# Kernel optimization log

Hardware: AMD Instinct MI355X
Metric: run time of the kernel (lower is better)

The kernel has to match this reference:

```python
import jax, jax.numpy as jnp
import numpy as np

EPS = 1e-6

def _ln(x, g, b):
    m = x.mean(-1, keepdims=True)
    v = jnp.var(x, axis=-1, keepdims=True)
    return (x - m) * jax.lax.rsqrt(v + EPS) * g + b

def _mha(x, qkv_w, out_w, out_b, heads, dh):
    # vit-style attention: Linear(dim, 3*heads*dh, bias=False), chunk into q,k,v
    B, N, _ = x.shape
    qkv = (x @ qkv_w).reshape(B, N, 3, heads, dh).transpose(2, 0, 3, 1, 4)
    q, k, v = qkv[0], qkv[1], qkv[2]                       # [B,H,N,dh]
    attn = jax.nn.softmax(jnp.einsum('bhid,bhjd->bhij', q, k) * (dh ** -0.5), axis=-1)
    o = jnp.einsum('bhij,bhjd->bhid', attn, v).transpose(0, 2, 1, 3).reshape(B, N, heads * dh)
    return o @ out_w + out_b

def _tx(x, p, heads, dh):
    # standard prenorm transformer stack, p = stacked per-layer params
    (l1g, l1b, qw, ow, ob, l2g, l2b, f1w, f1b, f2w, f2b, ng, nb) = p
    for i in range(l1g.shape[0]):
        x = x + _mha(_ln(x, l1g[i], l1b[i]), qw[i], ow[i], ob[i], heads, dh)
        h = _ln(x, l2g[i], l2b[i])
        x = x + jax.nn.gelu(h @ f1w[i] + f1b[i]) @ f2w[i] + f2b[i]
    return _ln(x, ng, nb)

def _ats(x, l1g, l1b, qkvw, qkvb, projw, projb, l2g, l2b, f1w, f1b, f2w, f2b):
    # ATS block: attention + CLS-significance-driven adaptive token resampling (gather)
    B, N, D = x.shape
    heads = 6
    dh = D // heads
    h = _ln(x, l1g, l1b)
    qkv = (h @ qkvw + qkvb).reshape(B, N, 3, heads, dh).transpose(2, 0, 3, 1, 4)
    q, k, v = qkv[0], qkv[1], qkv[2]
    attn = jax.nn.softmax(jnp.einsum('bhid,bhjd->bhij', q, k) * (dh ** -0.5), axis=-1)  # [B,H,N,N]
    y = jnp.einsum('bhij,bhjd->bhid', attn, v).transpose(0, 2, 1, 3).reshape(B, N, D)
    y = y @ projw + projb
    # significance score: cls attention * value norm (ATS, Fayyaz et al.)
    vn = jnp.linalg.norm(v, axis=-1)                        # [B,H,N]
    s = (attn[:, :, 0, 1:] * vn[:, :, 1:]).mean(axis=1)     # [B,N-1]
    s = s / (s.sum(-1, keepdims=True) + 1e-8)
    cdf = jnp.cumsum(s, axis=-1)                            # [B,N-1]
    # deterministic inverse-transform sampling of N-1 tokens
    u = (jnp.arange(N - 1, dtype=x.dtype) + 0.5) / (N - 1)
    idx = jax.vmap(lambda c: jnp.searchsorted(c, u))(cdf)
    idx = jnp.clip(idx, 0, N - 2) + 1                       # skip cls slot
    idx = jnp.concatenate([jnp.zeros((B, 1), idx.dtype), idx], axis=1)  # keep cls
    g = lambda a: jnp.take_along_axis(a, idx[:, :, None], axis=1)
    x = g(x) + g(y)
    h = _ln(x, l2g, l2b)
    return x + jax.nn.gelu(h @ f1w + f1b) @ f2w + f2b

def reference(x, patch_w, patch_b, pos_emb, space_token, temporal_token,
              s_ln1_g, s_ln1_b, s_qkv_w, s_out_w, s_out_b, s_ln2_g, s_ln2_b,
              s_fc1_w, s_fc1_b, s_fc2_w, s_fc2_b, s_norm_g, s_norm_b,
              t_ln1_g, t_ln1_b, t_qkv_w, t_out_w, t_out_b, t_ln2_g, t_ln2_b,
              t_fc1_w, t_fc1_b, t_fc2_w, t_fc2_b, t_norm_g, t_norm_b,
              a_ln1_g, a_ln1_b, a_qkv_w, a_qkv_b, a_proj_w, a_proj_b,
              a_ln2_g, a_ln2_b, a_fc1_w, a_fc1_b, a_fc2_w, a_fc2_b,
              final_g, final_b, h1_w, h1_b, h2_w, h2_b):
    B, T = x.shape[0], x.shape[1]
    BT, D, P, HP = B * T, 192, 16, 14
    # patch embedding (conv16s16 as unfold + linear), channel-major flattening
    xt = x.reshape(BT, 3, HP, P, HP, P).transpose(0, 2, 4, 1, 3, 5).reshape(BT, HP * HP, 3 * P * P)
    xt = (xt @ patch_w + patch_b).reshape(B, T, HP * HP, D)
    cls = jnp.broadcast_to(space_token.reshape(1, 1, 1, D), (B, T, 1, D))
    xt = jnp.concatenate([cls, xt], axis=2) + pos_emb      # [B,T,197,D]
    xt = xt.reshape(BT, 197, D)
    xt = _tx(xt, (s_ln1_g, s_ln1_b, s_qkv_w, s_out_w, s_out_b, s_ln2_g, s_ln2_b,
                  s_fc1_w, s_fc1_b, s_fc2_w, s_fc2_b, s_norm_g, s_norm_b), 6, 64)
    for i in range(a_ln1_g.shape[0]):
        xt = _ats(xt, a_ln1_g[i], a_ln1_b[i], a_qkv_w[i], a_qkv_b[i], a_proj_w[i],
                  a_proj_b[i], a_ln2_g[i], a_ln2_b[i], a_fc1_w[i], a_fc1_b[i],
                  a_fc2_w[i], a_fc2_b[i])
    xc = xt[:, 0].reshape(B, T, D)
    tt = jnp.broadcast_to(temporal_token, (B, 1, D))
    xc = jnp.concatenate([tt, xc], axis=1)                 # [B,T+1,D]
    xc = _tx(xc, (t_ln1_g, t_ln1_b, t_qkv_w, t_out_w, t_out_b, t_ln2_g, t_ln2_b,
                  t_fc1_w, t_fc1_b, t_fc2_w, t_fc2_b, t_norm_g, t_norm_b), 6, 64)
    f = jnp.max(xc, axis=1)                                # AdaptiveMaxPool1d(1) over tokens
    f = _ln(f, final_g, final_b)
    return jax.nn.relu(f @ h1_w + h1_b) @ h2_w + h2_b      # mlp_head -> [B,2]

def setup_inputs():
    key = jax.random.key(0)
    ks = iter(jax.random.split(key, 64))
    def rn(shape, s=0.02):
        return jax.random.normal(next(ks), shape, dtype=jnp.float32) * s
    d = {}
    d['x'] = jax.random.normal(next(ks), (16, 5, 3, 224, 224), dtype=jnp.float32)
    d['patch_w'] = rn((768, 192)); d['patch_b'] = jnp.zeros((192,), jnp.float32)
    d['pos_emb'] = rn((1, 5, 197, 192))
    d['space_token'] = rn((1, 1, 192)); d['temporal_token'] = rn((1, 1, 192))
    def tx(depth, n):
        d[n + '_ln1_g'] = jnp.ones((depth, 192), jnp.float32); d[n + '_ln1_b'] = jnp.zeros((depth, 192), jnp.float32)
        d[n + '_qkv_w'] = rn((depth, 192, 1152)); d[n + '_out_w'] = rn((depth, 384, 192)); d[n + '_out_b'] = jnp.zeros((depth, 192), jnp.float32)
        d[n + '_ln2_g'] = jnp.ones((depth, 192), jnp.float32); d[n + '_ln2_b'] = jnp.zeros((depth, 192), jnp.float32)
        d[n + '_fc1_w'] = rn((depth, 192, 768)); d[n + '_fc1_b'] = jnp.zeros((depth, 768), jnp.float32)
        d[n + '_fc2_w'] = rn((depth, 768, 192)); d[n + '_fc2_b'] = jnp.zeros((depth, 192), jnp.float32)
        d[n + '_norm_g'] = jnp.ones((192,), jnp.float32); d[n + '_norm_b'] = jnp.zeros((192,), jnp.float32)
    tx(2, 's'); tx(3, 't')
    d['a_ln1_g'] = jnp.ones((12, 192), jnp.float32); d['a_ln1_b'] = jnp.zeros((12, 192), jnp.float32)
    d['a_qkv_w'] = rn((12, 192, 576)); d['a_qkv_b'] = jnp.zeros((12, 576), jnp.float32)
    d['a_proj_w'] = rn((12, 192, 192)); d['a_proj_b'] = jnp.zeros((12, 192), jnp.float32)
    d['a_ln2_g'] = jnp.ones((12, 192), jnp.float32); d['a_ln2_b'] = jnp.zeros((12, 192), jnp.float32)
    d['a_fc1_w'] = rn((12, 192, 768)); d['a_fc1_b'] = jnp.zeros((12, 768), jnp.float32)
    d['a_fc2_w'] = rn((12, 768, 192)); d['a_fc2_b'] = jnp.zeros((12, 192), jnp.float32)
    d['final_g'] = jnp.ones((192,), jnp.float32); d['final_b'] = jnp.zeros((192,), jnp.float32)
    d['h1_w'] = rn((192, 64)); d['h1_b'] = jnp.zeros((64,), jnp.float32)
    d['h2_w'] = rn((64, 2)); d['h2_b'] = jnp.zeros((2,), jnp.float32)
    return d
```

## Files before the change

### kernel.cpp

```cpp
#include <hip/hip_runtime.h>
#include <hip/hip_bf16.h>
#include <math.h>

typedef float in_t;
typedef float out_t;

__device__ __forceinline__ float ldi(const in_t* p, size_t i) { return (float)p[i]; }

#define DMODEL 192
#define NTOK   197
#define BT_    80
#define ROWS_  (BT_*NTOK)

__device__ __forceinline__ float gelu_f(float v) {
  return 0.5f*v*(1.f + tanhf(0.7978845608028654f*(v + 0.044715f*v*v*v)));
}

__device__ __forceinline__ short f2bf(float f) {
  union { float f; unsigned u; } v; v.f = f;
  unsigned r = v.u + 0x7FFFu + ((v.u >> 16) & 1u);
  return (short)(r >> 16);
}

typedef __attribute__((ext_vector_type(8))) short bfrag;
typedef __attribute__((ext_vector_type(4))) float f32x4;

__global__ __launch_bounds__(256)
void wconv_k(const float* __restrict__ W, short* __restrict__ O, int K, int N)
{
  __shared__ float tile[32][33];
  const int l = blockIdx.z;
  const int k0 = blockIdx.y*32, n0 = blockIdx.x*32;
  const float* Wl = W + (size_t)l*K*N;
  short* Ol = O + (size_t)l*K*N;
  const int tx = threadIdx.x & 31, ty = threadIdx.x >> 5;
  #pragma unroll
  for (int r = ty; r < 32; r += 8) {
    int k = k0 + r, n = n0 + tx;
    tile[r][tx] = (k < K && n < N) ? Wl[(size_t)k*N + n] : 0.f;
  }
  __syncthreads();
  #pragma unroll
  for (int r = ty; r < 32; r += 8) {
    int n = n0 + r, k = k0 + tx;
    if (n < N && k < K) Ol[(size_t)n*K + k] = f2bf(tile[tx][r]);
  }
}

template<int EPI, int ABF, int OBF>
__global__ __launch_bounds__(256)
void gemmW_k(const void* __restrict__ Ain, const short* __restrict__ Wt,
             const float* __restrict__ bias, const float* __restrict__ R,
             void* __restrict__ Cout, int M, int N, int K)
{
  constexpr int LP = 200;
  __shared__ short Asb[64][LP];
  __shared__ short Bsb[64][LP];
  const int t = threadIdx.x;
  const int w = t >> 6, lane = t & 63;
  const int bm0 = blockIdx.y*64, bn0 = blockIdx.x*64;
  const int sr = t >> 2;
  const int sk = (t & 3) * 8;
  f32x4 acc[4] = {};

  for (int k0 = 0; k0 < K; k0 += 192) {
    const int gm = bm0 + sr;
    #pragma unroll
    for (int cc = 0; cc < 6; ++cc) {
      const int kk = cc*32 + sk;
      short y[8] = {0,0,0,0,0,0,0,0};
      if (gm < M) {
        if (ABF == 0) {
          const float* ap = (const float*)Ain + (size_t)gm*K + k0 + kk;
          float4 v0 = *(const float4*)ap;
          float4 v1 = *(const float4*)(ap + 4);
          y[0]=f2bf(v0.x); y[1]=f2bf(v0.y); y[2]=f2bf(v0.z); y[3]=f2bf(v0.w);
          y[4]=f2bf(v1.x); y[5]=f2bf(v1.y); y[6]=f2bf(v1.z); y[7]=f2bf(v1.w);
        } else {
          *(bfrag*)y = *(const bfrag*)((const short*)Ain + (size_t)gm*K + k0 + kk);
        }
      }
      *(bfrag*)&Asb[sr][kk] = *(bfrag*)y;
      bfrag bv = *(const bfrag*)(Wt + (size_t)(bn0 + sr)*K + k0 + kk);
      *(bfrag*)&Bsb[sr][kk] = bv;
    }
    __syncthreads();
    const int fr = lane & 15, g8 = (lane >> 4) * 8;
    #pragma unroll
    for (int ks = 0; ks < 6; ++ks) {
      bfrag af = *(const bfrag*)&Asb[w*16 + fr][ks*32 + g8];
      #pragma unroll
      for (int nt = 0; nt < 4; ++nt) {
        bfrag bf = *(const bfrag*)&Bsb[nt*16 + fr][ks*32 + g8];
        acc[nt] = __builtin_amdgcn_mfma_f32_16x16x32_bf16(af, bf, acc[nt], 0, 0, 0);
      }
    }
    __syncthreads();
  }
  const int col = lane & 15, rg = (lane >> 4) * 4;
  #pragma unroll
  for (int nt = 0; nt < 4; ++nt) {
    int gn = bn0 + nt*16 + col;
    float bv = bias ? bias[gn] : 0.f;
    #pragma unroll
    for (int r = 0; r < 4; ++r) {
      int gm = bm0 + w*16 + rg + r;
      if (gm < M) {
        float v = acc[nt][r] + bv;
        if (EPI==1) v = gelu_f(v);
        if (EPI==2) v += R[(size_t)gm*N + gn];
        if (OBF) ((short*)Cout)[(size_t)gm*N + gn] = f2bf(v);
        else     ((float*)Cout)[(size_t)gm*N + gn] = v;
      }
    }
  }
}

__global__ __launch_bounds__(256)
void ln_k(const float* __restrict__ x, const in_t* __restrict__ g, const in_t* __restrict__ b,
          float* __restrict__ o, int rows)
{
  int t = threadIdx.x, wave = t>>6, lane = t&63;
  int r = blockIdx.x*4 + wave;
  if (r >= rows) return;
  const float* xr = x + (size_t)r*DMODEL;
  float e0 = xr[lane], e1 = xr[lane+64], e2 = xr[lane+128];
  float s = e0+e1+e2;
  #pragma unroll
  for (int off=32; off; off>>=1) s += __shfl_xor(s, off);
  float mean = s / 192.f;
  float d0=e0-mean, d1=e1-mean, d2=e2-mean;
  float v = d0*d0+d1*d1+d2*d2;
  #pragma unroll
  for (int off=32; off; off>>=1) v += __shfl_xor(v, off);
  float rs = 1.f / sqrtf(v/192.f + 1e-6f);
  float* orow = o + (size_t)r*DMODEL;
  orow[lane]     = d0*rs*ldi(g,lane)     + ldi(b,lane);
  orow[lane+64]  = d1*rs*ldi(g,lane+64)  + ldi(b,lane+64);
  orow[lane+128] = d2*rs*ldi(g,lane+128) + ldi(b,lane+128);
}

template<int DH, int W>
__global__ __launch_bounds__(W*64)
void attnM_k(const float* __restrict__ qkv, short* __restrict__ out,
             float* __restrict__ attn0, int heads, float scale)
{
  constexpr int NSEQ = 197;
  constexpr int NP   = 224;
  constexpr int KG   = DH/8;
  constexpr int CT   = DH/16;
  constexpr int NF   = DH/32;
  __shared__ short Kb[KG][NP][8];
  __shared__ short Vt[NP/8][DH][8];
  __shared__ short Ps[W][NP/8][16][8];

  const int bh = blockIdx.x;
  const int b = bh / heads, h = bh - b*heads;
  const int stride = 3*heads*DH;
  const float* __restrict__ base = qkv + (size_t)b*NSEQ*stride;
  const int qo = h*DH, ko = heads*DH + h*DH, vo = 2*heads*DH + h*DH;
  const int t = threadIdx.x, w = t>>6, lane = t&63;

  for (int idx = t; idx < NP*DH; idx += W*64) {
    int j = idx / DH, d = idx - j*DH;
    float kv = 0.f, vv = 0.f;
    if (j < NSEQ) {
      kv = base[(size_t)j*stride + ko + d];
      vv = base[(size_t)j*stride + vo + d];
    }
    Kb[d>>3][j][d&7] = f2bf(kv);
    Vt[j>>3][d][j&7] = f2bf(vv);
  }
  __syncthreads();

  const int c = lane & 15, g = lane >> 4, rg = g*4;
  const float NEG = -3.0e38f;

  for (int st = w; st < 13; st += W) {
    const int q0 = st*16;
    int qrow = q0 + c; if (qrow > NSEQ-1) qrow = NSEQ-1;
    bfrag aq[NF];
    {
      const float* qp = base + (size_t)qrow*stride + qo + g*8;
      #pragma unroll
      for (int f = 0; f < NF; ++f) {
        float4 v0 = *(const float4*)(qp + f*32);
        float4 v1 = *(const float4*)(qp + f*32 + 4);
        short y[8] = {f2bf(v0.x),f2bf(v0.y),f2bf(v0.z),f2bf(v0.w),
                      f2bf(v1.x),f2bf(v1.y),f2bf(v1.z),f2bf(v1.w)};
        aq[f] = *(bfrag*)y;
      }
    }
    f32x4 sacc[14];
    #pragma unroll
    for (int jt = 0; jt < 14; ++jt) sacc[jt] = (f32x4){0.f,0.f,0.f,0.f};
    #pragma unroll
    for (int jt = 0; jt < 13; ++jt) {
      #pragma unroll
      for (int f = 0; f < NF; ++f) {
        bfrag bk = *(const bfrag*)&Kb[f*4 + g][jt*16 + c][0];
        sacc[jt] = __builtin_amdgcn_mfma_f32_16x16x32_bf16(aq[f], bk, sacc[jt], 0, 0, 0);
      }
    }
    float m0[4] = {NEG,NEG,NEG,NEG};
    #pragma unroll
    for (int jt = 0; jt < 14; ++jt) {
      const bool valid = (jt < 13) && (jt*16 + c < NSEQ);
      #pragma unroll
      for (int r = 0; r < 4; ++r) {
        float sv = valid ? sacc[jt][r]*scale : NEG;
        sacc[jt][r] = sv;
        m0[r] = fmaxf(m0[r], sv);
      }
    }
    #pragma unroll
    for (int off = 1; off < 16; off <<= 1)
      #pragma unroll
      for (int r = 0; r < 4; ++r) m0[r] = fmaxf(m0[r], __shfl_xor(m0[r], off));
    float sum[4] = {0.f,0.f,0.f,0.f};
    #pragma unroll
    for (int jt = 0; jt < 14; ++jt)
      #pragma unroll
      for (int r = 0; r < 4; ++r) {
        float e = expf(sacc[jt][r] - m0[r]);
        sacc[jt][r] = e;
        sum[r] += e;
      }
    #pragma unroll
    for (int off = 1; off < 16; off <<= 1)
      #pragma unroll
      for (int r = 0; r < 4; ++r) sum[r] += __shfl_xor(sum[r], off);
    float inv[4];
    #pragma unroll
    for (int r = 0; r < 4; ++r) inv[r] = 1.f / sum[r];

    if (attn0 != nullptr && st == 0 && g == 0) {
      #pragma unroll
      for (int jt = 0; jt < 13; ++jt) {
        int j = jt*16 + c;
        if (j < NSEQ) attn0[(size_t)bh*NSEQ + j] = sacc[jt][0]*inv[0];
      }
    }
    #pragma unroll
    for (int jt = 0; jt < 14; ++jt)
      #pragma unroll
      for (int r = 0; r < 4; ++r)
        Ps[w][jt*2 + (c>>3)][rg + r][c&7] = f2bf(sacc[jt][r]);
    f32x4 oacc[CT];
    #pragma unroll
    for (int ct = 0; ct < CT; ++ct) oacc[ct] = (f32x4){0.f,0.f,0.f,0.f};
    #pragma unroll
    for (int kc = 0; kc < 7; ++kc) {
      bfrag ap = *(const bfrag*)&Ps[w][kc*4 + g][c][0];
      #pragma unroll
      for (int ct = 0; ct < CT; ++ct) {
        bfrag bv = *(const bfrag*)&Vt[kc*4 + g][ct*16 + c][0];
        oacc[ct] = __builtin_amdgcn_mfma_f32_16x16x32_bf16(ap, bv, oacc[ct], 0, 0, 0);
      }
    }
    #pragma unroll
    for (int ct = 0; ct < CT; ++ct)
      #pragma unroll
      for (int r = 0; r < 4; ++r) {
        int q = q0 + rg + r;
        if (q < NSEQ)
          out[((size_t)b*NSEQ + q)*(size_t)(heads*DH) + h*DH + ct*16 + c] = f2bf(oacc[ct][r]*inv[r]);
      }
  }
}

template<int DH, int W>
__global__ __launch_bounds__(W*64)
void attn2r_k(const float* __restrict__ qkv, float* __restrict__ out,
              float* __restrict__ attn0, int Nseq, int heads, float scale)
{
  constexpr int QT = 8;
  constexpr int KTS = 204;
  constexpr int NPART = (DH == 64) ? 1 : 2;
  constexpr int DQ   = DH/4;
  constexpr int QPG  = 2;
  __shared__ float Kt[DH * KTS];
  __shared__ float Qt[W][DH][12];
  __shared__ float Ps[W][QT][200];

  const int bh = blockIdx.x;
  const int b = bh / heads, h = bh % heads;
  const int stride = 3 * heads * DH;
  const float* __restrict__ base = qkv + (size_t)b * Nseq * stride;
  const int qo = h * DH, ko = heads * DH + h * DH, vo = 2 * heads * DH + h * DH;
  const int t = threadIdx.x, w = t >> 6, lane = t & 63;

  for (int idx = t; idx < Nseq * DH; idx += W * 64) {
    int j = idx / DH, d0 = idx - j * DH;
    Kt[d0 * KTS + j] = base[(size_t)j * stride + ko + d0];
  }
  __syncthreads();

  const int d = lane & (DH - 1);
  const int nchunks = (Nseq + QT - 1) / QT;
  const int jcmax = (Nseq + 3) >> 2;
  const float NEG = -3.0e38f;
  const float4* Kt4 = (const float4*)Kt;

  const int part = (NPART == 2) ? (lane >> 5) : 0;
  const int qg   = (DH == 64) ? (lane >> 4) : ((lane >> 3) & 3);
  const int dq   = lane & (DQ - 1);
  const int dv   = 4 * dq;

  for (int ic = w; ic < nchunks; ic += W) {
    const int i0 = ic * QT;
    if ((DH == 64) || (lane >> 5) == 0) {
      #pragma unroll
      for (int q = 0; q < QT; ++q) {
        int i = i0 + q;
        Qt[w][d][q] = (i < Nseq) ? base[(size_t)i * stride + qo + d] : 0.f;
      }
    }
    float s[QT][4];
    #pragma unroll
    for (int q = 0; q < QT; ++q)
      #pragma unroll
      for (int u = 0; u < 4; ++u) s[q][u] = 0.f;
    #pragma unroll 4
    for (int dd = 0; dd < DH; ++dd) {
      float4 kv = (lane < 51) ? Kt4[dd * (KTS/4) + lane] : make_float4(0.f,0.f,0.f,0.f);
      float4 qA = *(const float4*)&Qt[w][dd][0];
      float4 qB = *(const float4*)&Qt[w][dd][4];
      float qv[8] = {qA.x, qA.y, qA.z, qA.w, qB.x, qB.y, qB.z, qB.w};
      float kr[4] = {kv.x, kv.y, kv.z, kv.w};
      #pragma unroll
      for (int q = 0; q < QT; ++q)
        #pragma unroll
        for (int u = 0; u < 4; ++u)
          s[q][u] = fmaf(qv[q], kr[u], s[q][u]);
    }
    float inv[QT];
    #pragma unroll
    for (int q = 0; q < QT; ++q) {
      float mx = NEG;
      #pragma unroll
      for (int u = 0; u < 4; ++u) {
        int j = 4*lane + u;
        s[q][u] = (j < Nseq) ? s[q][u]*scale : NEG;
        mx = fmaxf(mx, s[q][u]);
      }
      #pragma unroll
      for (int off = 32; off; off >>= 1) mx = fmaxf(mx, __shfl_xor(mx, off));
      float sum = 0.f;
      #pragma unroll
      for (int u = 0; u < 4; ++u) {
        float p = (4*lane + u < Nseq) ? expf(s[q][u] - mx) : 0.f;
        s[q][u] = p; sum += p;
      }
      #pragma unroll
      for (int off = 32; off; off >>= 1) sum += __shfl_xor(sum, off);
      inv[q] = 1.f / sum;
      if (lane < 50)
        *(float4*)&Ps[w][q][4*lane] = make_float4(s[q][0], s[q][1], s[q][2], s[q][3]);
    }
    if (attn0 != nullptr && i0 == 0) {
      #pragma unroll
      for (int u = 0; u < 4; ++u) {
        int j = 4*lane + u;
        if (j < Nseq) attn0[(size_t)bh*Nseq + j] = s[0][u]*inv[0];
      }
    }
    float o[QPG][4];
    #pragma unroll
    for (int qi = 0; qi < QPG; ++qi) { o[qi][0]=0.f; o[qi][1]=0.f; o[qi][2]=0.f; o[qi][3]=0.f; }
    const float* __restrict__ Vg = base + vo;
    for (int jc = part; jc < jcmax; jc += NPART) {
      const int jb = 4*jc;
      float4 V0 = make_float4(0.f,0.f,0.f,0.f), V1=V0, V2=V0, V3=V0;
      if (jb+0 < Nseq) V0 = *(const float4*)&Vg[(size_t)(jb+0)*stride + dv];
      if (jb+1 < Nseq) V1 = *(const float4*)&Vg[(size_t)(jb+1)*stride + dv];
      if (jb+2 < Nseq) V2 = *(const float4*)&Vg[(size_t)(jb+2)*stride + dv];
      if (jb+3 < Nseq) V3 = *(const float4*)&Vg[(size_t)(jb+3)*stride + dv];
      #pragma unroll
      for (int qi = 0; qi < QPG; ++qi) {
        float4 p4 = *(const float4*)&Ps[w][qg*QPG+qi][jb];
        o[qi][0] = fmaf(p4.w,V3.x, fmaf(p4.z,V2.x, fmaf(p4.y,V1.x, fmaf(p4.x,V0.x, o[qi][0]))));
        o[qi][1] = fmaf(p4.w,V3.y, fmaf(p4.z,V2.y, fmaf(p4.y,V1.y, fmaf(p4.x,V0.y, o[qi][1]))));
        o[qi][2] = fmaf(p4.w,V3.z, fmaf(p4.z,V2.z, fmaf(p4.y,V1.z, fmaf(p4.x,V0.z, o[qi][2]))));
        o[qi][3] = fmaf(p4.w,V3.w, fmaf(p4.z,V2.w, fmaf(p4.y,V1.w, fmaf(p4.x,V0.w, o[qi][3]))));
      }
    }
    if (NPART == 2) {
      #pragma unroll
      for (int qi = 0; qi < QPG; ++qi) {
        o[qi][0] += __shfl_xor(o[qi][0], 32);
        o[qi][1] += __shfl_xor(o[qi][1], 32);
        o[qi][2] += __shfl_xor(o[qi][2], 32);
        o[qi][3] += __shfl_xor(o[qi][3], 32);
      }
    }
    if (part == 0) {
      #pragma unroll
      for (int qi = 0; qi < QPG; ++qi) {
        float iv = inv[qi];
        if (qg == 1) iv = inv[QPG + qi];
        if (qg == 2) iv = inv[2*QPG + qi];
        if (qg == 3) iv = inv[3*QPG + qi];
        int i = i0 + qg*QPG + qi;
        if (i < Nseq) {
          float4 r = make_float4(o[qi][0]*iv, o[qi][1]*iv, o[qi][2]*iv, o[qi][3]*iv);
          *(float4*)&out[((size_t)b*Nseq + i)*(size_t)(heads*DH) + h*DH + dv] = r;
        }
      }
    }
  }
}

__global__ void patchify_k(const in_t* __restrict__ x, short* __restrict__ A)
{
  int idx = blockIdx.x*256 + threadIdx.x;
  const int total = BT_*196*768;
  if (idx >= total) return;
  int kc = idx % 768;
  int m  = idx / 768;
  int p  = m % 196;
  int bt = m / 196;
  int c  = kc >> 8;
  int py = (kc >> 4) & 15;
  int px = kc & 15;
  int ph = p / 14, pw = p % 14;
  size_t src = (((size_t)bt*3 + c)*224 + (ph*16+py))*224 + (pw*16+px);
  A[idx] = f2bf(ldi(x, src));
}

__global__ void assemble_k(const float* __restrict__ pt, const in_t* __restrict__ st,
                           const in_t* __restrict__ pe, float* __restrict__ X)
{
  int i = blockIdx.x*256 + threadIdx.x;
  const int total = BT_*NTOK*DMODEL;
  if (i >= total) return;
  int d  = i % DMODEL;
  int n  = (i / DMODEL) % NTOK;
  int bt = i / (DMODEL*NTOK);
  int tt = bt % 5;
  float base = (n == 0) ? ldi(st, d)
                        : pt[((size_t)bt*196 + (n-1))*DMODEL + d];
  X[i] = base + ldi(pe, ((size_t)tt*NTOK + n)*DMODEL + d);
}

__global__ void score_k(const float* __restrict__ attn0, const float* __restrict__ qkv,
                        float* __restrict__ S)
{
  int b = blockIdx.x;
  int jj = threadIdx.x;
  if (jj >= 196) return;
  int j = jj + 1;
  float acc = 0.f;
  #pragma unroll
  for (int h = 0; h < 6; ++h) {
    float a0 = attn0[((size_t)b*6 + h)*NTOK + j];
    const float* v = qkv + ((size_t)b*NTOK + j)*576 + 384 + h*32;
    float ss = 0.f;
    #pragma unroll
    for (int d = 0; d < 32; ++d) ss += v[d]*v[d];
    acc += a0 * sqrtf(ss);
  }
  S[(size_t)b*196 + jj] = acc / 6.0f;
}

__global__ void sample_k(const float* __restrict__ S, int* __restrict__ idxout)
{
  __shared__ float cdf[196];
  int b = blockIdx.x, t = threadIdx.x;
  if (t == 0) {
    float tot = 0.f;
    for (int k = 0; k < 196; ++k) tot += S[(size_t)b*196 + k];
    float denom = tot + 1e-8f;
    float run = 0.f;
    for (int k = 0; k < 196; ++k) { run += S[(size_t)b*196 + k] / denom; cdf[k] = run; }
    idxout[(size_t)b*NTOK] = 0;
  }
  __syncthreads();
  if (t < 196) {
    float u = ((float)t + 0.5f) / 196.0f;
    int cnt = 0;
    for (int k = 0; k < 196; ++k) cnt += (cdf[k] < u) ? 1 : 0;
    int c = cnt > 195 ? 195 : cnt;
    idxout[(size_t)b*NTOK + 1 + t] = c + 1;
  }
}

__global__ void gather_k(const float* __restrict__ X, const float* __restrict__ P,
                         const int* __restrict__ idx, float* __restrict__ Xo)
{
  int i = blockIdx.x*256 + threadIdx.x;
  const int total = BT_*NTOK*DMODEL;
  if (i >= total) return;
  int d  = i % DMODEL;
  int n  = (i / DMODEL) % NTOK;
  int bt = i / (DMODEL*NTOK);
  int src = idx[(size_t)bt*NTOK + n];
  size_t sr = ((size_t)bt*NTOK + src)*DMODEL + d;
  Xo[i] = X[sr] + P[sr];
}

__global__ void build_xc_k(const float* __restrict__ X, const in_t* __restrict__ tt,
                           float* __restrict__ xc)
{
  int i = blockIdx.x*256 + threadIdx.x;
  const int total = 16*6*DMODEL;
  if (i >= total) return;
  int d = i % DMODEL;
  int n = (i / DMODEL) % 6;
  int b = i / (DMODEL*6);
  xc[i] = (n == 0) ? ldi(tt, d)
                   : X[(((size_t)b*5 + (n-1))*NTOK + 0)*DMODEL + d];
}

__global__ __launch_bounds__(256)
void head_k(const float* __restrict__ xc, const in_t* __restrict__ fg, const in_t* __restrict__ fb,
            const in_t* __restrict__ w1, const in_t* __restrict__ b1,
            const in_t* __restrict__ w2, const in_t* __restrict__ b2,
            out_t* __restrict__ outp)
{
  __shared__ float fn[DMODEL];
  __shared__ float hid[64];
  __shared__ float mv[2];
  int b = blockIdx.x, t = threadIdx.x;
  if (t < DMODEL) {
    float m = xc[((size_t)b*6 + 0)*DMODEL + t];
    #pragma unroll
    for (int n = 1; n < 6; ++n) m = fmaxf(m, xc[((size_t)b*6 + n)*DMODEL + t]);
    fn[t] = m;
  }
  __syncthreads();
  if (t == 0) {
    float s = 0.f;
    for (int d = 0; d < DMODEL; ++d) s += fn[d];
    float mean = s / 192.f;
    float v = 0.f;
    for (int d = 0; d < DMODEL; ++d) { float dd = fn[d]-mean; v += dd*dd; }
    mv[0] = mean; mv[1] = 1.f / sqrtf(v/192.f + 1e-6f);
  }
  __syncthreads();
  if (t < DMODEL) fn[t] = (fn[t]-mv[0])*mv[1]*ldi(fg,t) + ldi(fb,t);
  __syncthreads();
  if (t < 64) {
    float a = ldi(b1, t);
    for (int d = 0; d < DMODEL; ++d) a += fn[d]*ldi(w1, (size_t)d*64 + t);
    hid[t] = fmaxf(a, 0.f);
  }
  __syncthreads();
  if (t < 2) {
    float a = ldi(b2, t);
    for (int j = 0; j < 64; ++j) a += hid[j]*ldi(w2, (size_t)j*2 + t);
    outp[(size_t)b*2 + t] = (out_t)a;
  }
}

extern "C" void kernel_launch(void* const* d_in, const int* in_sizes, int n_in,
                              void* d_out, int out_size, void* d_ws, size_t ws_size,
                              hipStream_t stream)
{
  if (n_in < 50) return;
  const in_t* x_in     = (const in_t*)d_in[0];
  const in_t* patch_w  = (const in_t*)d_in[1];
  const in_t* patch_b  = (const in_t*)d_in[2];
  const in_t* pos_emb  = (const in_t*)d_in[3];
  const in_t* space_tk = (const in_t*)d_in[4];
  const in_t* temp_tk  = (const in_t*)d_in[5];
  const in_t* s_ln1_g = (const in_t*)d_in[6];  const in_t* s_ln1_b = (const in_t*)d_in[7];
  const in_t* s_qkv_w = (const in_t*)d_in[8];  const in_t* s_out_w = (const in_t*)d_in[9];
  const in_t* s_out_b = (const in_t*)d_in[10]; const in_t* s_ln2_g = (const in_t*)d_in[11];
  const in_t* s_ln2_b = (const in_t*)d_in[12]; const in_t* s_fc1_w = (const in_t*)d_in[13];
  const in_t* s_fc1_b = (const in_t*)d_in[14]; const in_t* s_fc2_w = (const in_t*)d_in[15];
  const in_t* s_fc2_b = (const in_t*)d_in[16]; const in_t* s_nrm_g = (const in_t*)d_in[17];
  const in_t* s_nrm_b = (const in_t*)d_in[18];
  const in_t* t_ln1_g = (const in_t*)d_in[19]; const in_t* t_ln1_b = (const in_t*)d_in[20];
  const in_t* t_qkv_w = (const in_t*)d_in[21]; const in_t* t_out_w = (const in_t*)d_in[22];
  const in_t* t_out_b = (const in_t*)d_in[23]; const in_t* t_ln2_g = (const in_t*)d_in[24];
  const in_t* t_ln2_b = (const in_t*)d_in[25]; const in_t* t_fc1_w = (const in_t*)d_in[26];
  const in_t* t_fc1_b = (const in_t*)d_in[27]; const in_t* t_fc2_w = (const in_t*)d_in[28];
  const in_t* t_fc2_b = (const in_t*)d_in[29]; const in_t* t_nrm_g = (const in_t*)d_in[30];
  const in_t* t_nrm_b = (const in_t*)d_in[31];
  const in_t* a_ln1_g = (const in_t*)d_in[32]; const in_t* a_ln1_b = (const in_t*)d_in[33];
  const in_t* a_qkv_w = (const in_t*)d_in[34]; const in_t* a_qkv_b = (const in_t*)d_in[35];
  const in_t* a_prj_w = (const in_t*)d_in[36]; const in_t* a_prj_b = (const in_t*)d_in[37];
  const in_t* a_ln2_g = (const in_t*)d_in[38]; const in_t* a_ln2_b = (const in_t*)d_in[39];
  const in_t* a_fc1_w = (const in_t*)d_in[40]; const in_t* a_fc1_b = (const in_t*)d_in[41];
  const in_t* a_fc2_w = (const in_t*)d_in[42]; const in_t* a_fc2_b = (const in_t*)d_in[43];
  const in_t* final_g = (const in_t*)d_in[44]; const in_t* final_b = (const in_t*)d_in[45];
  const in_t* h1_w = (const in_t*)d_in[46];    const in_t* h1_b = (const in_t*)d_in[47];
  const in_t* h2_w = (const in_t*)d_in[48];    const in_t* h2_b = (const in_t*)d_in[49];

  float* ws = (float*)d_ws;
  size_t off = 0;
  auto alloc = [&](size_t nf) { size_t r = off; off += (nf + 63) & ~((size_t)63); return r; };
  size_t oX    = alloc((size_t)ROWS_*DMODEL);
  size_t oX2   = alloc((size_t)ROWS_*DMODEL);
  size_t oH    = alloc((size_t)ROWS_*DMODEL);
  size_t oQKV  = alloc((size_t)ROWS_*1152);
  size_t oY    = alloc((size_t)ROWS_*384);
  size_t oA0   = alloc((size_t)480*NTOK);
  size_t oSB   = alloc((size_t)BT_*196);
  size_t oXC   = alloc((size_t)16*6*DMODEL);
  size_t oIDX  = alloc((size_t)BT_*NTOK);
  size_t oFFt  = alloc((size_t)96*768);
  size_t oWB   = alloc((size_t)4202496 + 64);
  size_t oYb   = alloc((size_t)ROWS_*384/2 + 64);
  size_t oFFb  = alloc((size_t)ROWS_*768/2 + 64);
  if (ws_size < off*sizeof(float)) return;

  float* X   = ws + oX;
  float* X2  = ws + oX2;
  float* H   = ws + oH;
  float* QKV = ws + oQKV;
  float* Y   = ws + oY;
  float* A0  = ws + oA0;
  float* SB  = ws + oSB;
  float* XC  = ws + oXC;
  int*   IDX = (int*)(ws + oIDX);
  float* FFt = ws + oFFt;
  short* WB  = (short*)(ws + oWB);
  short* Yb  = (short*)(ws + oYb);
  short* FFb = (short*)(ws + oFFb);

  size_t wo = 0;
  auto wslot = [&](size_t n){ size_t r = wo; wo += n; return r; };
  size_t wPatch = wslot(147456);
  size_t wSqkv  = wslot(442368);
  size_t wSout  = wslot(147456);
  size_t wSfc1  = wslot(294912);
  size_t wSfc2  = wslot(294912);
  size_t wAqkv  = wslot(1327104);
  size_t wAprj  = wslot(442368);
  size_t wAfc1  = wslot(1769472);
  size_t wAfc2  = wslot(1769472);
  size_t wTqkv  = wslot(663552);
  size_t wTout  = wslot(221184);
  size_t wTfc1  = wslot(442368);
  size_t wTfc2  = wslot(442368);

  auto wconv = [&](const in_t* W, size_t slot, int K, int N, int L) {
    dim3 g(N/32, K/32, L);
    hipLaunchKernelGGL(wconv_k, g, dim3(256), 0, stream, W, WB + slot, K, N);
  };
  wconv(patch_w, wPatch, 768, 192, 1);
  wconv(s_qkv_w, wSqkv, 192, 1152, 2);
  wconv(s_out_w, wSout, 384, 192, 2);
  wconv(s_fc1_w, wSfc1, 192, 768, 2);
  wconv(s_fc2_w, wSfc2, 768, 192, 2);
  wconv(a_qkv_w, wAqkv, 192, 576, 12);
  wconv(a_prj_w, wAprj, 192, 192, 12);
  wconv(a_fc1_w, wAfc1, 192, 768, 12);
  wconv(a_fc2_w, wAfc2, 768, 192, 12);
  wconv(t_qkv_w, wTqkv, 192, 1152, 3);
  wconv(t_out_w, wTout, 384, 192, 3);
  wconv(t_fc1_w, wTfc1, 192, 768, 3);
  wconv(t_fc2_w, wTfc2, 768, 192, 3);

  auto gemm = [&](int epi, int abf, int obf, const void* A, const short* Wt,
                  const float* bias, const float* R, void* C, int M, int N, int K) {
    dim3 grid(N/64, (M+63)/64);
    if (epi==0 && abf==0)              hipLaunchKernelGGL((gemmW_k<0,0,0>), grid, dim3(256), 0, stream, A, Wt, bias, R, C, M, N, K);
    else if (epi==0 && abf==1)         hipLaunchKernelGGL((gemmW_k<0,1,0>), grid, dim3(256), 0, stream, A, Wt, bias, R, C, M, N, K);
    else if (epi==1 && obf==1)         hipLaunchKernelGGL((gemmW_k<1,0,1>), grid, dim3(256), 0, stream, A, Wt, bias, R, C, M, N, K);
    else if (epi==1)                   hipLaunchKernelGGL((gemmW_k<1,0,0>), grid, dim3(256), 0, stream, A, Wt, bias, R, C, M, N, K);
    else if (epi==2 && abf==1)         hipLaunchKernelGGL((gemmW_k<2,1,0>), grid, dim3(256), 0, stream, A, Wt, bias, R, C, M, N, K);
    else                               hipLaunchKernelGGL((gemmW_k<2,0,0>), grid, dim3(256), 0, stream, A, Wt, bias, R, C, M, N, K);
  };
  auto ln = [&](const float* xi, const in_t* g, const in_t* b, float* o, int rows) {
    hipLaunchKernelGGL(ln_k, dim3((rows+3)/4), dim3(256), 0, stream, xi, g, b, o, rows);
  };

  {
    int total = BT_*196*768;
    hipLaunchKernelGGL(patchify_k, dim3((total+255)/256), dim3(256), 0, stream, x_in, FFb);
    gemm(0, 1, 0, FFb, WB + wPatch, patch_b, nullptr, Y, 15680, 192, 768);
    int tot2 = BT_*NTOK*DMODEL;
    hipLaunchKernelGGL(assemble_k, dim3((tot2+255)/256), dim3(256), 0, stream, Y, space_tk, pos_emb, X);
  }

  const float sc64 = 0.125f;
  const float sc32 = 0.17677669529663687f;

  for (int i = 0; i < 2; ++i) {
    ln(X, s_ln1_g + (size_t)i*192, s_ln1_b + (size_t)i*192, H, ROWS_);
    gemm(0, 0, 0, H, WB + wSqkv + (size_t)i*192*1152, nullptr, nullptr, QKV, ROWS_, 1152, 192);
    hipLaunchKernelGGL((attnM_k<64,8>), dim3(BT_*6), dim3(512), 0, stream, QKV, Yb, (float*)nullptr, 6, sc64);
    gemm(2, 1, 0, Yb, WB + wSout + (size_t)i*384*192, s_out_b + (size_t)i*192, X, X, ROWS_, 192, 384);
    ln(X, s_ln2_g + (size_t)i*192, s_ln2_b + (size_t)i*192, H, ROWS_);
    gemm(1, 0, 1, H, WB + wSfc1 + (size_t)i*192*768, s_fc1_b + (size_t)i*768, nullptr, FFb, ROWS_, 768, 192);
    gemm(2, 1, 0, FFb, WB + wSfc2 + (size_t)i*768*192, s_fc2_b + (size_t)i*192, X, X, ROWS_, 192, 768);
  }
  ln(X, s_nrm_g, s_nrm_b, X, ROWS_);

  float* xa = X; float* xb = X2;
  for (int i = 0; i < 12; ++i) {
    ln(xa, a_ln1_g + (size_t)i*192, a_ln1_b + (size_t)i*192, H, ROWS_);
    gemm(0, 0, 0, H, WB + wAqkv + (size_t)i*192*576, a_qkv_b + (size_t)i*576, nullptr, QKV, ROWS_, 576, 192);
    hipLaunchKernelGGL((attnM_k<32,4>), dim3(BT_*6), dim3(256), 0, stream, QKV, Yb, A0, 6, sc32);
    gemm(0, 1, 0, Yb, WB + wAprj + (size_t)i*192*192, a_prj_b + (size_t)i*192, nullptr, H, ROWS_, 192, 192);
    hipLaunchKernelGGL(score_k, dim3(BT_), dim3(256), 0, stream, A0, QKV, SB);
    hipLaunchKernelGGL(sample_k, dim3(BT_), dim3(256), 0, stream, SB, IDX);
    {
      int tot = BT_*NTOK*DMODEL;
      hipLaunchKernelGGL(gather_k, dim3((tot+255)/256), dim3(256), 0, stream, xa, H, IDX, xb);
    }
    ln(xb, a_ln2_g + (size_t)i*192, a_ln2_b + (size_t)i*192, H, ROWS_);
    gemm(1, 0, 1, H, WB + wAfc1 + (size_t)i*192*768, a_fc1_b + (size_t)i*768, nullptr, FFb, ROWS_, 768, 192);
    gemm(2, 1, 0, FFb, WB + wAfc2 + (size_t)i*768*192, a_fc2_b + (size_t)i*192, xb, xb, ROWS_, 192, 768);
    float* tmp = xa; xa = xb; xb = tmp;
  }

  {
    int tot = 16*6*DMODEL;
    hipLaunchKernelGGL(build_xc_k, dim3((tot+255)/256), dim3(256), 0, stream, xa, temp_tk, XC);
  }
  const int MT = 16*6;
  for (int i = 0; i < 3; ++i) {
    ln(XC, t_ln1_g + (size_t)i*192, t_ln1_b + (size_t)i*192, H, MT);
    gemm(0, 0, 0, H, WB + wTqkv + (size_t)i*192*1152, nullptr, nullptr, QKV, MT, 1152, 192);
    hipLaunchKernelGGL((attn2r_k<64,8>), dim3(16*6), dim3(512), 0, stream, QKV, Y, (float*)nullptr, 6, 6, sc64);
    gemm(2, 0, 0, Y, WB + wTout + (size_t)i*384*192, t_out_b + (size_t)i*192, XC, XC, MT, 192, 384);
    ln(XC, t_ln2_g + (size_t)i*192, t_ln2_b + (size_t)i*192, H, MT);
    gemm(1, 0, 0, H, WB + wTfc1 + (size_t)i*192*768, t_fc1_b + (size_t)i*768, nullptr, FFt, MT, 768, 192);
    gemm(2, 0, 0, FFt, WB + wTfc2 + (size_t)i*768*192, t_fc2_b + (size_t)i*192, XC, XC, MT, 192, 768);
  }
  ln(XC, t_nrm_g, t_nrm_b, XC, MT);

  hipLaunchKernelGGL(head_k, dim3(16), dim3(256), 0, stream, XC, final_g, final_b,
                     h1_w, h1_b, h2_w, h2_b, (out_t*)d_out);
}
```

Baseline: 2.830 ms.

## Emit bf16 QKV from GEMM, fuse score+sample and gather+layernorm kernels

The QKV GEMMs now write bf16 output. In the ATS blocks the output is split into a bf16 Q/K buffer plus an fp32 V buffer, so the attention kernel loads K and Q as 8-wide bf16 vectors instead of converting fp32 per element. The score and sampling kernels are merged into one kernel, and the token gather is fused with the following layernorm, removing launches and a full activation round trip. Q and K are now rounded to bf16 before the attention kernel rather than inside it, which the old kernel also did, so precision is unchanged. The spatial-stage V is also bf16.

```diff
diff --git a/kernel.cpp b/kernel.cpp
--- a/kernel.cpp
+++ b/kernel.cpp
@@ -51,7 +51,8 @@
 __global__ __launch_bounds__(256)
 void gemmW_k(const void* __restrict__ Ain, const short* __restrict__ Wt,
              const float* __restrict__ bias, const float* __restrict__ R,
-             void* __restrict__ Cout, int M, int N, int K)
+             void* __restrict__ Cout, float* __restrict__ Cout2,
+             int M, int N, int K)
 {
   constexpr int LP = 200;
   __shared__ short Asb[64][LP];
@@ -109,8 +110,12 @@
         float v = acc[nt][r] + bv;
         if (EPI==1) v = gelu_f(v);
         if (EPI==2) v += R[(size_t)gm*N + gn];
-        if (OBF) ((short*)Cout)[(size_t)gm*N + gn] = f2bf(v);
-        else     ((float*)Cout)[(size_t)gm*N + gn] = v;
+        if (OBF==0)      ((float*)Cout)[(size_t)gm*N + gn] = v;
+        else if (OBF==1) ((short*)Cout)[(size_t)gm*N + gn] = f2bf(v);
+        else {
+          if (gn < 384) ((short*)Cout)[(size_t)gm*384 + gn] = f2bf(v);
+          else          Cout2[(size_t)gm*192 + (gn - 384)] = v;
+        }
       }
     }
   }
@@ -140,10 +145,43 @@
   orow[lane+128] = d2*rs*ldi(g,lane+128) + ldi(b,lane+128);
 }
 
-template<int DH, int W>
+__global__ __launch_bounds__(256)
+void gatherln_k(const float* __restrict__ X, const float* __restrict__ P,
+                const int* __restrict__ idx, const in_t* __restrict__ g,
+                const in_t* __restrict__ b, float* __restrict__ Xo,
+                float* __restrict__ H2, int rows)
+{
+  int t = threadIdx.x, wave = t>>6, lane = t&63;
+  int r = blockIdx.x*4 + wave;
+  if (r >= rows) return;
+  int bt = r / NTOK, n = r - bt*NTOK;
+  int src = idx[(size_t)bt*NTOK + n];
+  size_t sb = ((size_t)bt*NTOK + src)*DMODEL;
+  float e0 = X[sb+lane]     + P[sb+lane];
+  float e1 = X[sb+lane+64]  + P[sb+lane+64];
+  float e2 = X[sb+lane+128] + P[sb+lane+128];
+  float* xr = Xo + (size_t)r*DMODEL;
+  xr[lane] = e0; xr[lane+64] = e1; xr[lane+128] = e2;
+  float s = e0+e1+e2;
+  #pragma unroll
+  for (int off=32; off; off>>=1) s += __shfl_xor(s, off);
+  float mean = s / 192.f;
+  float d0=e0-mean, d1=e1-mean, d2=e2-mean;
+  float v = d0*d0+d1*d1+d2*d2;
+  #pragma unroll
+  for (int off=32; off; off>>=1) v += __shfl_xor(v, off);
+  float rs = 1.f / sqrtf(v/192.f + 1e-6f);
+  float* orow = H2 + (size_t)r*DMODEL;
+  orow[lane]     = d0*rs*ldi(g,lane)     + ldi(b,lane);
+  orow[lane+64]  = d1*rs*ldi(g,lane+64)  + ldi(b,lane+64);
+  orow[lane+128] = d2*rs*ldi(g,lane+128) + ldi(b,lane+128);
+}
+
+template<int DH, int W, int MODE>
 __global__ __launch_bounds__(W*64)
-void attnM_k(const float* __restrict__ qkv, short* __restrict__ out,
-             float* __restrict__ attn0, int heads, float scale)
+void attnB_k(const short* __restrict__ qk, const float* __restrict__ vf,
+             short* __restrict__ out, float* __restrict__ attn0,
+             int heads, float scale)
 {
   constexpr int NSEQ = 197;
   constexpr int NP   = 224;
@@ -156,20 +194,31 @@
 
   const int bh = blockIdx.x;
   const int b = bh / heads, h = bh - b*heads;
-  const int stride = 3*heads*DH;
-  const float* __restrict__ base = qkv + (size_t)b*NSEQ*stride;
-  const int qo = h*DH, ko = heads*DH + h*DH, vo = 2*heads*DH + h*DH;
+  const int qks = ((MODE==1) ? 3 : 2)*heads*DH;
+  const short* __restrict__ baseqk = qk + (size_t)b*NSEQ*qks;
+  const int qo = h*DH, ko = heads*DH + h*DH;
+  const int vs = heads*DH;
+  const float* __restrict__ basev = (MODE==2) ? (vf + (size_t)b*NSEQ*vs) : nullptr;
+  const int vo = (MODE==1) ? (2*heads*DH + h*DH) : (h*DH);
   const int t = threadIdx.x, w = t>>6, lane = t&63;
 
+  {
+    short z8[8] = {0,0,0,0,0,0,0,0};
+    for (int idx = t; idx < NP*KG; idx += W*64) {
+      int j = idx / KG, dg = idx - j*KG;
+      bfrag kv = *(bfrag*)z8;
+      if (j < NSEQ) kv = *(const bfrag*)(baseqk + (size_t)j*qks + ko + dg*8);
+      *(bfrag*)&Kb[dg][j][0] = kv;
+    }
+  }
   for (int idx = t; idx < NP*DH; idx += W*64) {
     int j = idx / DH, d = idx - j*DH;
-    float kv = 0.f, vv = 0.f;
+    short vv = 0;
     if (j < NSEQ) {
-      kv = base[(size_t)j*stride + ko + d];
-      vv = base[(size_t)j*stride + vo + d];
-    }
-    Kb[d>>3][j][d&7] = f2bf(kv);
-    Vt[j>>3][d][j&7] = f2bf(vv);
+      if (MODE==1) vv = baseqk[(size_t)j*qks + vo + d];
+      else         vv = f2bf(basev[(size_t)j*vs + vo + d]);
+    }
+    Vt[j>>3][d][j&7] = vv;
   }
   __syncthreads();
 
@@ -181,15 +230,9 @@
     int qrow = q0 + c; if (qrow > NSEQ-1) qrow = NSEQ-1;
     bfrag aq[NF];
     {
-      const float* qp = base + (size_t)qrow*stride + qo + g*8;
-      #pragma unroll
-      for (int f = 0; f < NF; ++f) {
-        float4 v0 = *(const float4*)(qp + f*32);
-        float4 v1 = *(const float4*)(qp + f*32 + 4);
-        short y[8] = {f2bf(v0.x),f2bf(v0.y),f2bf(v0.z),f2bf(v0.w),
-                      f2bf(v1.x),f2bf(v1.y),f2bf(v1.z),f2bf(v1.w)};
-        aq[f] = *(bfrag*)y;
-      }
+      const short* qp = baseqk + (size_t)qrow*qks + qo + g*8;
+      #pragma unroll
+      for (int f = 0; f < NF; ++f) aq[f] = *(const bfrag*)(qp + f*32);
     }
     f32x4 sacc[14];
     #pragma unroll
@@ -443,36 +486,34 @@
   X[i] = base + ldi(pe, ((size_t)tt*NTOK + n)*DMODEL + d);
 }
 
-__global__ void score_k(const float* __restrict__ attn0, const float* __restrict__ qkv,
-                        float* __restrict__ S)
-{
-  int b = blockIdx.x;
-  int jj = threadIdx.x;
-  if (jj >= 196) return;
-  int j = jj + 1;
-  float acc = 0.f;
-  #pragma unroll
-  for (int h = 0; h < 6; ++h) {
-    float a0 = attn0[((size_t)b*6 + h)*NTOK + j];
-    const float* v = qkv + ((size_t)b*NTOK + j)*576 + 384 + h*32;
-    float ss = 0.f;
-    #pragma unroll
-    for (int d = 0; d < 32; ++d) ss += v[d]*v[d];
-    acc += a0 * sqrtf(ss);
-  }
-  S[(size_t)b*196 + jj] = acc / 6.0f;
-}
-
-__global__ void sample_k(const float* __restrict__ S, int* __restrict__ idxout)
-{
+__global__ __launch_bounds__(256)
+void scoresample_k(const float* __restrict__ attn0, const float* __restrict__ Vf,
+                   int* __restrict__ idxout)
+{
+  __shared__ float S[196];
   __shared__ float cdf[196];
   int b = blockIdx.x, t = threadIdx.x;
+  if (t < 196) {
+    int j = t + 1;
+    float acc = 0.f;
+    #pragma unroll
+    for (int h = 0; h < 6; ++h) {
+      float a0 = attn0[((size_t)b*6 + h)*NTOK + j];
+      const float* v = Vf + ((size_t)b*NTOK + j)*192 + h*32;
+      float ss = 0.f;
+      #pragma unroll
+      for (int d = 0; d < 32; ++d) ss += v[d]*v[d];
+      acc += a0 * sqrtf(ss);
+    }
+    S[t] = acc / 6.0f;
+  }
+  __syncthreads();
   if (t == 0) {
     float tot = 0.f;
-    for (int k = 0; k < 196; ++k) tot += S[(size_t)b*196 + k];
+    for (int k = 0; k < 196; ++k) tot += S[k];
     float denom = tot + 1e-8f;
     float run = 0.f;
-    for (int k = 0; k < 196; ++k) { run += S[(size_t)b*196 + k] / denom; cdf[k] = run; }
+    for (int k = 0; k < 196; ++k) { run += S[k] / denom; cdf[k] = run; }
     idxout[(size_t)b*NTOK] = 0;
   }
   __syncthreads();
@@ -483,20 +524,6 @@
     int c = cnt > 195 ? 195 : cnt;
     idxout[(size_t)b*NTOK + 1 + t] = c + 1;
   }
-}
-
-__global__ void gather_k(const float* __restrict__ X, const float* __restrict__ P,
-                         const int* __restrict__ idx, float* __restrict__ Xo)
-{
-  int i = blockIdx.x*256 + threadIdx.x;
-  const int total = BT_*NTOK*DMODEL;
-  if (i >= total) return;
-  int d  = i % DMODEL;
-  int n  = (i / DMODEL) % NTOK;
-  int bt = i / (DMODEL*NTOK);
-  int src = idx[(size_t)bt*NTOK + n];
-  size_t sr = ((size_t)bt*NTOK + src)*DMODEL + d;
-  Xo[i] = X[sr] + P[sr];
 }
 
 __global__ void build_xc_k(const float* __restrict__ X, const in_t* __restrict__ tt,
@@ -594,31 +621,35 @@
   size_t oX    = alloc((size_t)ROWS_*DMODEL);
   size_t oX2   = alloc((size_t)ROWS_*DMODEL);
   size_t oH    = alloc((size_t)ROWS_*DMODEL);
-  size_t oQKV  = alloc((size_t)ROWS_*1152);
+  size_t oH2   = alloc((size_t)ROWS_*DMODEL);
   size_t oY    = alloc((size_t)ROWS_*384);
+  size_t oVf   = alloc((size_t)ROWS_*192);
   size_t oA0   = alloc((size_t)480*NTOK);
-  size_t oSB   = alloc((size_t)BT_*196);
   size_t oXC   = alloc((size_t)16*6*DMODEL);
   size_t oIDX  = alloc((size_t)BT_*NTOK);
+  size_t oQKVt = alloc((size_t)96*1152);
   size_t oFFt  = alloc((size_t)96*768);
   size_t oWB   = alloc((size_t)4202496 + 64);
+  size_t oQKVb = alloc((size_t)ROWS_*1152/2 + 64);
   size_t oYb   = alloc((size_t)ROWS_*384/2 + 64);
   size_t oFFb  = alloc((size_t)ROWS_*768/2 + 64);
   if (ws_size < off*sizeof(float)) return;
 
-  float* X   = ws + oX;
-  float* X2  = ws + oX2;
-  float* H   = ws + oH;
-  float* QKV = ws + oQKV;
-  float* Y   = ws + oY;
-  float* A0  = ws + oA0;
-  float* SB  = ws + oSB;
-  float* XC  = ws + oXC;
-  int*   IDX = (int*)(ws + oIDX);
-  float* FFt = ws + oFFt;
-  short* WB  = (short*)(ws + oWB);
-  short* Yb  = (short*)(ws + oYb);
-  short* FFb = (short*)(ws + oFFb);
+  float* X    = ws + oX;
+  float* X2   = ws + oX2;
+  float* H    = ws + oH;
+  float* H2   = ws + oH2;
+  float* Y    = ws + oY;
+  float* Vf   = ws + oVf;
+  float* A0   = ws + oA0;
+  float* XC   = ws + oXC;
+  int*   IDX  = (int*)(ws + oIDX);
+  float* QKVt = ws + oQKVt;
+  float* FFt  = ws + oFFt;
+  short* WB   = (short*)(ws + oWB);
+  short* QKVb = (short*)(ws + oQKVb);
+  short* Yb   = (short*)(ws + oYb);
+  short* FFb  = (short*)(ws + oFFb);
 
   size_t wo = 0;
   auto wslot = [&](size_t n){ size_t r = wo; wo += n; return r; };
@@ -655,14 +686,17 @@
   wconv(t_fc2_w, wTfc2, 768, 192, 3);
 
   auto gemm = [&](int epi, int abf, int obf, const void* A, const short* Wt,
-                  const float* bias, const float* R, void* C, int M, int N, int K) {
+                  const float* bias, const float* R, void* C, float* C2,
+                  int M, int N, int K) {
     dim3 grid(N/64, (M+63)/64);
-    if (epi==0 && abf==0)              hipLaunchKernelGGL((gemmW_k<0,0,0>), grid, dim3(256), 0, stream, A, Wt, bias, R, C, M, N, K);
-    else if (epi==0 && abf==1)         hipLaunchKernelGGL((gemmW_k<0,1,0>), grid, dim3(256), 0, stream, A, Wt, bias, R, C, M, N, K);
-    else if (epi==1 && obf==1)         hipLaunchKernelGGL((gemmW_k<1,0,1>), grid, dim3(256), 0, stream, A, Wt, bias, R, C, M, N, K);
-    else if (epi==1)                   hipLaunchKernelGGL((gemmW_k<1,0,0>), grid, dim3(256), 0, stream, A, Wt, bias, R, C, M, N, K);
-    else if (epi==2 && abf==1)         hipLaunchKernelGGL((gemmW_k<2,1,0>), grid, dim3(256), 0, stream, A, Wt, bias, R, C, M, N, K);
-    else                               hipLaunchKernelGGL((gemmW_k<2,0,0>), grid, dim3(256), 0, stream, A, Wt, bias, R, C, M, N, K);
+    if (obf==2)                        hipLaunchKernelGGL((gemmW_k<0,0,2>), grid, dim3(256), 0, stream, A, Wt, bias, R, C, C2, M, N, K);
+    else if (epi==0 && abf==0 && obf==0) hipLaunchKernelGGL((gemmW_k<0,0,0>), grid, dim3(256), 0, stream, A, Wt, bias, R, C, C2, M, N, K);
+    else if (epi==0 && abf==0 && obf==1) hipLaunchKernelGGL((gemmW_k<0,0,1>), grid, dim3(256), 0, stream, A, Wt, bias, R, C, C2, M, N, K);
+    else if (epi==0 && abf==1 && obf==0) hipLaunchKernelGGL((gemmW_k<0,1,0>), grid, dim3(256), 0, stream, A, Wt, bias, R, C, C2, M, N, K);
+    else if (epi==1 && obf==1)         hipLaunchKernelGGL((gemmW_k<1,0,1>), grid, dim3(256), 0, stream, A, Wt, bias, R, C, C2, M, N, K);
+    else if (epi==1)                   hipLaunchKernelGGL((gemmW_k<1,0,0>), grid, dim3(256), 0, stream, A, Wt, bias, R, C, C2, M, N, K);
+    else if (epi==2 && abf==1)         hipLaunchKernelGGL((gemmW_k<2,1,0>), grid, dim3(256), 0, stream, A, Wt, bias, R, C, C2, M, N, K);
+    else                               hipLaunchKernelGGL((gemmW_k<2,0,0>), grid, dim3(256), 0, stream, A, Wt, bias, R, C, C2, M, N, K);
   };
   auto ln = [&](const float* xi, const in_t* g, const in_t* b, float* o, int rows) {
     hipLaunchKernelGGL(ln_k, dim3((rows+3)/4), dim3(256), 0, stream, xi, g, b, o, rows);
@@ -671,7 +705,7 @@
   {
     int total = BT_*196*768;
     hipLaunchKernelGGL(patchify_k, dim3((total+255)/256), dim3(256), 0, stream, x_in, FFb);
-    gemm(0, 1, 0, FFb, WB + wPatch, patch_b, nullptr, Y, 15680, 192, 768);
+    gemm(0, 1, 0, FFb, WB + wPatch, patch_b, nullptr, Y, nullptr, 15680, 192, 768);
     int tot2 = BT_*NTOK*DMODEL;
     hipLaunchKernelGGL(assemble_k, dim3((tot2+255)/256), dim3(256), 0, stream, Y, space_tk, pos_emb, X);
   }
@@ -681,30 +715,26 @@
 
   for (int i = 0; i < 2; ++i) {
     ln(X, s_ln1_g + (size_t)i*192, s_ln1_b + (size_t)i*192, H, ROWS_);
-    gemm(0, 0, 0, H, WB + wSqkv + (size_t)i*192*1152, nullptr, nullptr, QKV, ROWS_, 1152, 192);
-    hipLaunchKernelGGL((attnM_k<64,8>), dim3(BT_*6), dim3(512), 0, stream, QKV, Yb, (float*)nullptr, 6, sc64);
-    gemm(2, 1, 0, Yb, WB + wSout + (size_t)i*384*192, s_out_b + (size_t)i*192, X, X, ROWS_, 192, 384);
+    gemm(0, 0, 1, H, WB + wSqkv + (size_t)i*192*1152, nullptr, nullptr, QKVb, nullptr, ROWS_, 1152, 192);
+    hipLaunchKernelGGL((attnB_k<64,8,1>), dim3(BT_*6), dim3(512), 0, stream, QKVb, (const float*)nullptr, Yb, (float*)nullptr, 6, sc64);
+    gemm(2, 1, 0, Yb, WB + wSout + (size_t)i*384*192, s_out_b + (size_t)i*192, X, X, nullptr, ROWS_, 192, 384);
     ln(X, s_ln2_g + (size_t)i*192, s_ln2_b + (size_t)i*192, H, ROWS_);
-    gemm(1, 0, 1, H, WB + wSfc1 + (size_t)i*192*768, s_fc1_b + (size_t)i*768, nullptr, FFb, ROWS_, 768, 192);
-    gemm(2, 1, 0, FFb, WB + wSfc2 + (size_t)i*768*192, s_fc2_b + (size_t)i*192, X, X, ROWS_, 192, 768);
+    gemm(1, 0, 1, H, WB + wSfc1 + (size_t)i*192*768, s_fc1_b + (size_t)i*768, nullptr, FFb, nullptr, ROWS_, 768, 192);
+    gemm(2, 1, 0, FFb, WB + wSfc2 + (size_t)i*768*192, s_fc2_b + (size_t)i*192, X, X, nullptr, ROWS_, 192, 768);
   }
   ln(X, s_nrm_g, s_nrm_b, X, ROWS_);
 
   float* xa = X; float* xb = X2;
   for (int i = 0; i < 12; ++i) {
     ln(xa, a_ln1_g + (size_t)i*192, a_ln1_b + (size_t)i*192, H, ROWS_);
-    gemm(0, 0, 0, H, WB + wAqkv + (size_t)i*192*576, a_qkv_b + (size_t)i*576, nullptr, QKV, ROWS_, 576, 192);
-    hipLaunchKernelGGL((attnM_k<32,4>), dim3(BT_*6), dim3(256), 0, stream, QKV, Yb, A0, 6, sc32);
-    gemm(0, 1, 0, Yb, WB + wAprj + (size_t)i*192*192, a_prj_b + (size_t)i*192, nullptr, H, ROWS_, 192, 192);
-    hipLaunchKernelGGL(score_k, dim3(BT_), dim3(256), 0, stream, A0, QKV, SB);
-    hipLaunchKernelGGL(sample_k, dim3(BT_), dim3(256), 0, stream, SB, IDX);
-    {
-      int tot = BT_*NTOK*DMODEL;
-      hipLaunchKernelGGL(gather_k, dim3((tot+255)/256), dim3(256), 0, stream, xa, H, IDX, xb);
-    }
-    ln(xb, a_ln2_g + (size_t)i*192, a_ln2_b + (size_t)i*192, H, ROWS_);
-    gemm(1, 0, 1, H, WB + wAfc1 + (size_t)i*192*768, a_fc1_b + (size_t)i*768, nullptr, FFb, ROWS_, 768, 192);
-    gemm(2, 1, 0, FFb, WB + wAfc2 + (size_t)i*768*192, a_fc2_b + (size_t)i*192, xb, xb, ROWS_, 192, 768);
+    gemm(0, 0, 2, H, WB + wAqkv + (size_t)i*192*576, a_qkv_b + (size_t)i*576, nullptr, QKVb, Vf, ROWS_, 576, 192);
+    hipLaunchKernelGGL((attnB_k<32,4,2>), dim3(BT_*6), dim3(256), 0, stream, QKVb, Vf, Yb, A0, 6, sc32);
+    gemm(0, 1, 0, Yb, WB + wAprj + (size_t)i*192*192, a_prj_b + (size_t)i*192, nullptr, H, nullptr, ROWS_, 192, 192);
+    hipLaunchKernelGGL(scoresample_k, dim3(BT_), dim3(256), 0, stream, A0, Vf, IDX);
+    hipLaunchKernelGGL(gatherln_k, dim3((ROWS_+3)/4), dim3(256), 0, stream,
+                       xa, H, IDX, a_ln2_g + (size_t)i*192, a_ln2_b + (size_t)i*192, xb, H2, ROWS_);
+    gemm(1, 0, 1, H2, WB + wAfc1 + (size_t)i*192*768, a_fc1_b + (size_t)i*768, nullptr, FFb, nullptr, ROWS_, 768, 192);
+    gemm(2, 1, 0, FFb, WB + wAfc2 + (size_t)i*768*192, a_fc2_b + (size_t)i*192, xb, xb, nullptr, ROWS_, 192, 768);
     float* tmp = xa; xa = xb; xb = tmp;
   }
 
@@ -715,12 +745,12 @@
   const int MT = 16*6;
   for (int i = 0; i < 3; ++i) {
     ln(XC, t_ln1_g + (size_t)i*192, t_ln1_b + (size_t)i*192, H, MT);
-    gemm(0, 0, 0, H, WB + wTqkv + (size_t)i*192*1152, nullptr, nullptr, QKV, MT, 1152, 192);
-    hipLaunchKernelGGL((attn2r_k<64,8>), dim3(16*6), dim3(512), 0, stream, QKV, Y, (float*)nullptr, 6, 6, sc64);
-    gemm(2, 0, 0, Y, WB + wTout + (size_t)i*384*192, t_out_b + (size_t)i*192, XC, XC, MT, 192, 384);
+    gemm(0, 0, 0, H, WB + wTqkv + (size_t)i*192*1152, nullptr, nullptr, QKVt, nullptr, MT, 1152, 192);
+    hipLaunchKernelGGL((attn2r_k<64,8>), dim3(16*6), dim3(512), 0, stream, QKVt, Y, (float*)nullptr, 6, 6, sc64);
+    gemm(2, 0, 0, Y, WB + wTout + (size_t)i*384*192, t_out_b + (size_t)i*192, XC, XC, nullptr, MT, 192, 384);
     ln(XC, t_ln2_g + (size_t)i*192, t_ln2_b + (size_t)i*192, H, MT);
-    gemm(1, 0, 0, H, WB + wTfc1 + (size_t)i*192*768, t_fc1_b + (size_t)i*768, nullptr, FFt, MT, 768, 192);
-    gemm(2, 0, 0, FFt, WB + wTfc2 + (size_t)i*768*192, t_fc2_b + (size_t)i*192, XC, XC, MT, 192, 768);
+    gemm(1, 0, 0, H, WB + wTfc1 + (size_t)i*192*768, t_fc1_b + (size_t)i*768, nullptr, FFt, nullptr, MT, 768, 192);
+    gemm(2, 0, 0, FFt, WB + wTfc2 + (size_t)i*768*192, t_fc2_b + (size_t)i*192, XC, XC, nullptr, MT, 192, 768);
   }
   ln(XC, t_nrm_g, t_nrm_b, XC, MT);
 
```

Result: faster. 2.673 ms (-5.6%).
